# Kernel tuning notes

Hardware: AMD Instinct MI355X
Metric: run time of the kernel (lower is better)

## Reference

```python
import jax, jax.numpy as jnp
import numpy as np

GROUPS = 8
EPS = 1e-5


def group_norm(x, gamma, beta):
    # x: (b, c, h, w); normalize per sample over each group of c//GROUPS channels and all spatial dims
    b, c, h, w = x.shape
    xg = x.reshape(b, GROUPS, c // GROUPS, h, w)
    mean = jnp.mean(xg, axis=(2, 3, 4), keepdims=True)
    var = jnp.var(xg, axis=(2, 3, 4), keepdims=True)
    xn = ((xg - mean) * jax.lax.rsqrt(var + EPS)).reshape(b, c, h, w)
    return xn * gamma[None, :, None, None] + beta[None, :, None, None]


def setup_inputs() -> dict:
    key = jax.random.key(0)
    k1, k2, k3 = jax.random.split(key, 3)
    b, c, h, w = 32, 256, 32, 32
    x = jax.random.normal(k1, (b, c, h, w), dtype=jnp.float32)
    qkv_w = jax.random.normal(k2, (3 * c, c), dtype=jnp.float32) * 0.02
    qkv_b = jnp.zeros((3 * c,), dtype=jnp.float32)
    out_w = jax.random.normal(k3, (c, c), dtype=jnp.float32) * 0.02
    out_b = jnp.zeros((c,), dtype=jnp.float32)
    gn_gamma = jnp.ones((c,), dtype=jnp.float32)
    gn_beta = jnp.zeros((c,), dtype=jnp.float32)
    return {"x": x, "gn_gamma": gn_gamma, "gn_beta": gn_beta,
            "qkv_w": qkv_w, "qkv_b": qkv_b, "out_w": out_w, "out_b": out_b}


def reference(x, gn_gamma, gn_beta, qkv_w, qkv_b, out_w, out_b):
    b, c, h, w = x.shape
    xn = group_norm(x, gn_gamma, gn_beta)
    # 1x1 conv == per-pixel linear: (b,c,h,w) x (3c,c) -> (b,3c,h,w)
    qkv = jnp.einsum('bchw,dc->bdhw', xn, qkv_w) + qkv_b[None, :, None, None]
    q, k, v = jnp.split(qkv, 3, axis=1)
    # (b, c, h, w) -> (b, hw, c)
    def tok(t):
        return t.transpose(0, 2, 3, 1).reshape(b, h * w, c)
    q, k, v = tok(q), tok(k), tok(v)
    scale = 1.0 / jnp.sqrt(jnp.asarray(c, dtype=x.dtype))
    scores = jnp.einsum('bnc,bmc->bnm', q, k) * scale  # (b, hw, hw)
    attn = jax.nn.softmax(scores, axis=-1)
    out = jnp.einsum('bnm,bmc->bnc', attn, v)  # (b, hw, c)
    out = out.reshape(b, h, w, c).transpose(0, 3, 1, 2)  # (b, c, h, w)
    out = jnp.einsum('bchw,dc->bdhw', out, out_w) + out_b[None, :, None, None]
    return out + x
```

## Files before the change

kernel.cpp:

```cpp
#include <hip/hip_runtime.h>
#include <hip/hip_bf16.h>
#include <stdint.h>


typedef __bf16 bf16_t;
typedef __bf16 bf16x4 __attribute__((ext_vector_type(4)));
typedef __bf16 bf16x8 __attribute__((ext_vector_type(8)));
typedef float f32x4 __attribute__((ext_vector_type(4)));
typedef float f32x16 __attribute__((ext_vector_type(16)));
typedef _Float16 f16x4 __attribute__((ext_vector_type(4)));

#define MFMA32(a, b, c) __builtin_amdgcn_mfma_f32_32x32x16_bf16((a), (b), (c), 0, 0, 0)
#define GLL16(g, l)                                                                     \
    __builtin_amdgcn_global_load_lds((const __attribute__((address_space(1))) void*)(g), \
                                     (__attribute__((address_space(3))) void*)(l), 16, 0, 0)
#define WAITV8 asm volatile("s_waitcnt vmcnt(8)" ::: "memory")
#define WAITV0 asm volatile("s_waitcnt vmcnt(0)" ::: "memory")
#define WLG0   asm volatile("s_waitcnt lgkmcnt(0)" ::: "memory")
#define SBAR   __builtin_amdgcn_s_barrier()
#define SCH0   __builtin_amdgcn_sched_barrier(0)

#define QSCALE 0.0901684400555f

__device__ inline uint32_t pack2(float a, float b) {
    union { uint32_t u; __bf16 h[2]; } w;
    w.h[0] = (__bf16)a; w.h[1] = (__bf16)b;
    return w.u;
}

__global__ void cast_bf16(const float* __restrict__ s, bf16_t* __restrict__ d, int n) {
    for (int i = blockIdx.x * blockDim.x + threadIdx.x; i < n; i += gridDim.x * blockDim.x)
        d[i] = (bf16_t)s[i];
}

__global__ __launch_bounds__(256) void gn_kernel(const float* __restrict__ x,
                                                 const float* __restrict__ gamma,
                                                 const float* __restrict__ beta,
                                                 bf16_t* __restrict__ xn) {
    extern __shared__ char gsm[];
    float* red = (float*)(gsm + 65536);
    int bg = blockIdx.x, b = bg >> 3, g = bg & 7;
    const float* base = x + (size_t)(b * 256 + g * 32) * 1024;
    int tid = threadIdx.x;

    float s = 0.f, ss = 0.f;
    #pragma unroll 4
    for (int c = 0; c < 32; c++) {
        float4 v = *(const float4*)(base + c * 1024 + tid * 4);
        s += v.x + v.y + v.z + v.w;
        ss += v.x * v.x + v.y * v.y + v.z * v.z + v.w * v.w;
        f16x4 h = {(_Float16)v.x, (_Float16)v.y, (_Float16)v.z, (_Float16)v.w};
        *(f16x4*)(gsm + c * 2048 + ((tid * 8) ^ ((c & 7) << 4))) = h;
    }
    for (int off = 32; off; off >>= 1) { s += __shfl_down(s, off); ss += __shfl_down(ss, off); }
    if ((tid & 63) == 0) { red[tid >> 6] = s; red[4 + (tid >> 6)] = ss; }
    __syncthreads();
    float S = red[0] + red[1] + red[2] + red[3];
    float SS = red[4] + red[5] + red[6] + red[7];
    float mean = S * (1.0f / 32768.0f);
    float var = SS * (1.0f / 32768.0f) - mean * mean;
    float rstd = rsqrtf(var + 1e-5f);

    int c = tid & 31;
    float gam = gamma[g * 32 + c] * rstd;
    float bet = beta[g * 32 + c] - mean * gam;
    bf16_t* dst = xn + (size_t)(b * 1024) * 256 + g * 32 + c;
    #pragma unroll 4
    for (int it = 0; it < 128; it++) {
        int p = it * 8 + (tid >> 5);
        _Float16 hv = *(_Float16*)(gsm + c * 2048 + ((p * 2) ^ ((c & 7) << 4)));
        dst[(size_t)p * 256] = (bf16_t)((float)hv * gam + bet);
    }
}

__device__ inline void stage128(const char* src, char* dstLDS, int wv, int lane) {
    int r2 = lane >> 5, u = lane & 31;
    #pragma unroll
    for (int t = 0; t < 16; t++) {
        int row = t * 8 + wv * 2 + r2;
        GLL16(src + (size_t)row * 512 + ((u ^ (row & 7)) * 16), dstLDS + (t * 8 + wv * 2) * 512);
    }
}
__device__ inline bf16x8 lds_frag(const char* base, int row, int sl) {
    return *(const bf16x8*)(base + row * 512 + ((sl ^ (row & 7)) * 16));
}

__global__ __launch_bounds__(256) void gemm_qk(const bf16_t* __restrict__ xn,
                                               const bf16_t* __restrict__ wq,
                                               const float* __restrict__ qkv_b,
                                               bf16_t* __restrict__ qb,
                                               bf16_t* __restrict__ kb) {
    extern __shared__ char smem[];
    char* As = smem; char* Bs = smem + 65536;
    int tid = threadIdx.x, wv = tid >> 6, lane = tid & 63;
    int m0 = blockIdx.x * 128, n0 = blockIdx.y * 128;
    stage128((const char*)xn + (size_t)m0 * 512, As, wv, lane);
    stage128((const char*)wq + (size_t)n0 * 512, Bs, wv, lane);
    __syncthreads();

    int wr = wv >> 1, wc = wv & 1, l31 = lane & 31, hi = lane >> 5;
    f32x16 acc[2][2] = {};
    #pragma unroll
    for (int ks = 0; ks < 16; ks++) {
        int sl = ks * 2 + hi;
        bf16x8 a0 = lds_frag(As, wr * 64 + l31, sl);
        bf16x8 a1 = lds_frag(As, wr * 64 + 32 + l31, sl);
        bf16x8 b0 = lds_frag(Bs, wc * 64 + l31, sl);
        bf16x8 b1 = lds_frag(Bs, wc * 64 + 32 + l31, sl);
        acc[0][0] = MFMA32(a0, b0, acc[0][0]);
        acc[0][1] = MFMA32(a0, b1, acc[0][1]);
        acc[1][0] = MFMA32(a1, b0, acc[1][0]);
        acc[1][1] = MFMA32(a1, b1, acc[1][1]);
    }
    #pragma unroll
    for (int ms = 0; ms < 2; ms++)
        #pragma unroll
        for (int ns = 0; ns < 2; ns++) {
            int n = n0 + wc * 64 + ns * 32 + l31;
            float bias = qkv_b[n];
            bool isq = n < 256;
            float sc = isq ? QSCALE : 1.0f;
            bf16_t* dst = isq ? qb : kb;
            int d = isq ? n : n - 256;
            #pragma unroll
            for (int r = 0; r < 16; r++) {
                int m = m0 + wr * 64 + ms * 32 + (r & 3) + 8 * (r >> 2) + 4 * hi;
                dst[(size_t)m * 256 + d] = (bf16_t)((acc[ms][ns][r] + bias) * sc);
            }
        }
}

__global__ __launch_bounds__(256) void gemm_v(const bf16_t* __restrict__ xn,
                                              const bf16_t* __restrict__ wq,
                                              const float* __restrict__ qkv_b,
                                              bf16_t* __restrict__ vt) {
    extern __shared__ char smem[];
    char* As = smem; char* Bs = smem + 65536;
    int tid = threadIdx.x, wv = tid >> 6, lane = tid & 63;
    int d0 = blockIdx.x * 128, t0 = blockIdx.y * 128;
    stage128((const char*)wq + (size_t)(512 + d0) * 512, As, wv, lane);
    stage128((const char*)xn + (size_t)t0 * 512, Bs, wv, lane);
    __syncthreads();

    int wr = wv >> 1, wc = wv & 1, l31 = lane & 31, hi = lane >> 5;
    f32x16 acc[2][2] = {};
    #pragma unroll
    for (int ks = 0; ks < 16; ks++) {
        int sl = ks * 2 + hi;
        bf16x8 a0 = lds_frag(As, wr * 64 + l31, sl);
        bf16x8 a1 = lds_frag(As, wr * 64 + 32 + l31, sl);
        bf16x8 b0 = lds_frag(Bs, wc * 64 + l31, sl);
        bf16x8 b1 = lds_frag(Bs, wc * 64 + 32 + l31, sl);
        acc[0][0] = MFMA32(a0, b0, acc[0][0]);
        acc[0][1] = MFMA32(a0, b1, acc[0][1]);
        acc[1][0] = MFMA32(a1, b0, acc[1][0]);
        acc[1][1] = MFMA32(a1, b1, acc[1][1]);
    }
    #pragma unroll
    for (int ms = 0; ms < 2; ms++)
        #pragma unroll
        for (int ns = 0; ns < 2; ns++) {
            int tok0 = t0 + wc * 64 + ns * 32;
            #pragma unroll
            for (int r = 0; r < 16; r++) {
                int d = d0 + wr * 64 + ms * 32 + (r & 3) + 8 * (r >> 2) + 4 * hi;
                int tok = tok0 + l31;
                int bb = tok >> 10, pos = tok & 1023;
                vt[(size_t)bb * 262144 + (size_t)d * 1024 + pos] =
                    (bf16_t)(acc[ms][ns][r] + qkv_b[512 + d]);
            }
        }
}

__global__ __launch_bounds__(256) void gemm_out(const bf16_t* __restrict__ wo,
                                                const bf16_t* __restrict__ ao,
                                                const float* __restrict__ out_b,
                                                const float* __restrict__ x,
                                                float* __restrict__ out) {
    extern __shared__ char smem[];
    char* As = smem; char* Bs = smem + 65536;
    int tid = threadIdx.x, wv = tid >> 6, lane = tid & 63;
    int c0 = blockIdx.x * 128, t0 = blockIdx.y * 128;
    stage128((const char*)wo + (size_t)c0 * 512, As, wv, lane);
    stage128((const char*)ao + (size_t)t0 * 512, Bs, wv, lane);
    __syncthreads();

    int wr = wv >> 1, wc = wv & 1, l31 = lane & 31, hi = lane >> 5;
    f32x16 acc[2][2] = {};
    #pragma unroll
    for (int ks = 0; ks < 16; ks++) {
        int sl = ks * 2 + hi;
        bf16x8 a0 = lds_frag(As, wr * 64 + l31, sl);
        bf16x8 a1 = lds_frag(As, wr * 64 + 32 + l31, sl);
        bf16x8 b0 = lds_frag(Bs, wc * 64 + l31, sl);
        bf16x8 b1 = lds_frag(Bs, wc * 64 + 32 + l31, sl);
        acc[0][0] = MFMA32(a0, b0, acc[0][0]);
        acc[0][1] = MFMA32(a0, b1, acc[0][1]);
        acc[1][0] = MFMA32(a1, b0, acc[1][0]);
        acc[1][1] = MFMA32(a1, b1, acc[1][1]);
    }
    #pragma unroll
    for (int ms = 0; ms < 2; ms++)
        #pragma unroll
        for (int ns = 0; ns < 2; ns++) {
            #pragma unroll
            for (int r = 0; r < 16; r++) {
                int c = c0 + wr * 64 + ms * 32 + (r & 3) + 8 * (r >> 2) + 4 * hi;
                int tok = t0 + wc * 64 + ns * 32 + l31;
                int bb = tok >> 10, pos = tok & 1023;
                size_t idx = ((size_t)bb * 256 + c) * 1024 + pos;
                out[idx] = acc[ms][ns][r] + out_b[c] + x[idx];
            }
        }
}

__global__ __launch_bounds__(256, 1) void attn_kernel(const bf16_t* __restrict__ qb,
                                                      const bf16_t* __restrict__ kb,
                                                      const bf16_t* __restrict__ vt,
                                                      bf16_t* __restrict__ ao) {
    extern __shared__ char smem[];
    int tid = threadIdx.x, i = blockIdx.x;
    int b = (i & 7) + ((i >> 6) << 3);
    int qt = (i >> 3) & 7;
    int wv = tid >> 6, lane = tid & 63, l31 = lane & 31, hi = lane >> 5;

    const char* kbase = (const char*)kb + (size_t)b * 524288;
    const char* vbase = (const char*)vt + (size_t)b * 524288;

    int qg = qt * 128 + wv * 32 + l31;
    const char* qsrc = (const char*)qb + (size_t)(b * 1024 + qg) * 512;
    bf16x8 qf[16];
    #pragma unroll
    for (int ks = 0; ks < 16; ks++) qf[ks] = *(const bf16x8*)(qsrc + ks * 32 + hi * 16);

    f32x16 o[8] = {};
    f32x16 sp0 = {}, sp1 = {};
    float mrun = -1e30f, lrun = 0.f;

    auto stage_K = [&](int ch) {
        char* Kd = smem + (ch & 1) * 32768;
        int j0 = ch * 64;
        #pragma unroll
        for (int t = 0; t < 8; t++) {
            int r0 = wv * 16 + t * 2;
            int r = r0 + (lane >> 5), u = lane & 31;
            GLL16(kbase + (size_t)(j0 + r) * 512 + ((u ^ (r & 7)) * 16), Kd + r0 * 512);
        }
    };
    auto stage_V = [&](int ch) {
        char* Vd = smem + 65536 + (ch & 1) * 32768;
        int j0 = ch * 64;
        #pragma unroll
        for (int t = 0; t < 8; t++) {
            int r0 = wv * 64 + t * 8;
            int r = r0 + (lane >> 3), u = lane & 7;
            GLL16(vbase + (size_t)r * 2048 + j0 * 2 + ((u ^ (r & 7)) * 16), Vd + r0 * 128);
        }
    };
    auto qkt = [&](int ch, f32x16& s0, f32x16& s1) {
        const char* Ks = smem + (ch & 1) * 32768;
        #pragma unroll
        for (int ks = 0; ks < 16; ks++) {
            int col = ks * 32 + hi * 16;
            bf16x8 k0 = *(const bf16x8*)(Ks + l31 * 512 + (col ^ ((l31 & 7) << 4)));
            bf16x8 k1 = *(const bf16x8*)(Ks + (32 + l31) * 512 + (col ^ ((l31 & 7) << 4)));
            s0 = MFMA32(k0, qf[ks], s0);
            s1 = MFMA32(k1, qf[ks], s1);
        }
    };
    auto smax_pv = [&](int ch) {
        float mc = -1e30f;
        #pragma unroll
        for (int r = 0; r < 16; r++) mc = fmaxf(mc, fmaxf(sp0[r], sp1[r]));
        mc = fmaxf(mc, __shfl_xor(mc, 32));
        float mo = mrun;
        float mn = (mc <= mo + 8.0f) ? mo : mc;
        float rs = 0.f;
        #pragma unroll
        for (int r = 0; r < 16; r++) {
            sp0[r] = exp2f(sp0[r] - mn);
            sp1[r] = exp2f(sp1[r] - mn);
            rs += sp0[r] + sp1[r];
        }
        rs += __shfl_xor(rs, 32);
        float al = exp2f(mo - mn);
        lrun = lrun * al + rs;
        mrun = mn;
        if (__any(mn != mo)) {
            #pragma unroll
            for (int dt = 0; dt < 8; dt++) o[dt] = o[dt] * al;
        }
        const char* Vs = smem + 65536 + (ch & 1) * 32768;
        #pragma unroll
        for (int pk = 0; pk < 4; pk++) {
            float e0 = (pk < 2) ? sp0[(pk & 1) * 8 + 0] : sp1[(pk & 1) * 8 + 0];
            float e1 = (pk < 2) ? sp0[(pk & 1) * 8 + 1] : sp1[(pk & 1) * 8 + 1];
            float e2 = (pk < 2) ? sp0[(pk & 1) * 8 + 2] : sp1[(pk & 1) * 8 + 2];
            float e3 = (pk < 2) ? sp0[(pk & 1) * 8 + 3] : sp1[(pk & 1) * 8 + 3];
            float e4 = (pk < 2) ? sp0[(pk & 1) * 8 + 4] : sp1[(pk & 1) * 8 + 4];
            float e5 = (pk < 2) ? sp0[(pk & 1) * 8 + 5] : sp1[(pk & 1) * 8 + 5];
            float e6 = (pk < 2) ? sp0[(pk & 1) * 8 + 6] : sp1[(pk & 1) * 8 + 6];
            float e7 = (pk < 2) ? sp0[(pk & 1) * 8 + 7] : sp1[(pk & 1) * 8 + 7];
            uint32_t A0 = pack2(e0, e1), A1 = pack2(e2, e3);
            uint32_t B0 = pack2(e4, e5), B1 = pack2(e6, e7);
            asm volatile("v_permlane32_swap_b32 %0, %1" : "+v"(B0), "+v"(A0));
            asm volatile("v_permlane32_swap_b32 %0, %1" : "+v"(B1), "+v"(A1));
            union { bf16x8 v; uint32_t u[4]; } pw;
            pw.u[0] = A0; pw.u[1] = A1; pw.u[2] = B0; pw.u[3] = B1;
            #pragma unroll
            for (int dt = 0; dt < 8; dt++) {
                int d = dt * 32 + l31;
                bf16x8 vf =
                    *(const bf16x8*)(Vs + d * 128 + ((pk * 32 + hi * 16) ^ ((d & 7) << 4)));
                o[dt] = MFMA32(vf, pw.v, o[dt]);
            }
        }
    };

    stage_K(0); stage_V(0);
    WAITV8; SCH0; SBAR;
    stage_K(1);
    qkt(0, sp0, sp1);
    WLG0; SCH0; SBAR;
    stage_V(1);

    for (int ch = 1; ch < 16; ch++) {
        WAITV8; SCH0; SBAR;
        if (ch < 15) stage_K(ch + 1);
        f32x16 sn0 = {}, sn1 = {};
        qkt(ch, sn0, sn1);
        smax_pv(ch - 1);
        WLG0; SCH0; SBAR;
        if (ch < 15) stage_V(ch + 1);
        sp0 = sn0; sp1 = sn1;
    }
    WAITV0; SCH0; SBAR;
    smax_pv(15);

    float inv = 1.0f / lrun;
    char* aod = (char*)ao + (size_t)(b * 1024 + qg) * 512;
    #pragma unroll
    for (int dt = 0; dt < 8; dt++) {
        #pragma unroll
        for (int rg = 0; rg < 4; rg++) {
            bf16x4 w;
            #pragma unroll
            for (int r = 0; r < 4; r++) w[r] = (bf16_t)(o[dt][rg * 4 + r] * inv);
            *(bf16x4*)(aod + dt * 64 + rg * 16 + hi * 8) = w;
        }
    }
}

extern "C" void kernel_launch(void* const* d_in, const int* in_sizes, int n_in,
                              void* d_out, int out_size, void* d_ws, size_t ws_size,
                              hipStream_t stream) {
    (void)in_sizes; (void)n_in; (void)out_size; (void)ws_size;
    const float* x      = (const float*)d_in[0];
    const float* gamma  = (const float*)d_in[1];
    const float* beta   = (const float*)d_in[2];
    const float* qkv_w  = (const float*)d_in[3];
    const float* qkv_b  = (const float*)d_in[4];
    const float* out_w  = (const float*)d_in[5];
    const float* out_b  = (const float*)d_in[6];
    float* out = (float*)d_out;

    char* ws = (char*)d_ws;
    const size_t MB16 = 16777216;
    bf16_t* xn  = (bf16_t*)(ws);
    bf16_t* qb  = (bf16_t*)(ws + 1 * MB16);
    bf16_t* kb  = (bf16_t*)(ws + 2 * MB16);
    bf16_t* vt  = (bf16_t*)(ws + 3 * MB16);
    bf16_t* ao  = (bf16_t*)(ws + 4 * MB16);
    bf16_t* wqb = (bf16_t*)(ws + 5 * MB16);
    bf16_t* wob = (bf16_t*)(ws + 5 * MB16 + 393216);

    cast_bf16<<<192, 256, 0, stream>>>(qkv_w, wqb, 196608);
    cast_bf16<<<64, 256, 0, stream>>>(out_w, wob, 65536);
    gn_kernel<<<256, 256, 65600, stream>>>(x, gamma, beta, xn);
    gemm_qk<<<dim3(256, 4), 256, 131072, stream>>>(xn, wqb, qkv_b, qb, kb);
    gemm_v<<<dim3(2, 256), 256, 131072, stream>>>(xn, wqb, qkv_b, vt);
    attn_kernel<<<256, 256, 131072, stream>>>(qb, kb, vt, ao);
    gemm_out<<<dim3(2, 256), 256, 131072, stream>>>(wob, ao, out_b, x, out);
}
```

Before: 142.5 us.

## Fuse QKV GEMMs, restructure out GEMM, widen LDS swizzle, add MFMA priority

The separate Q/K and V projection kernels become one kernel per 128-token tile. It keeps the activation tile resident in LDS and streams double-buffered 64-row weight tiles. The output projection is restructured the same way, and the two weight casts are merged into one launch. LDS swizzles for K, V and the GEMMs change from 3-bit to 5-bit XOR patterns to reduce bank conflicts, and s_setprio brackets the MFMA loops. The goal is fewer launches, less redundant activation loading and fewer LDS conflicts. The cost is grids of only 256 blocks with one block per CU, plus serial per-block loops.

```diff
diff --git a/kernel.cpp b/kernel.cpp
--- a/kernel.cpp
+++ b/kernel.cpp
@@ -6,19 +6,17 @@
 typedef __bf16 bf16_t;
 typedef __bf16 bf16x4 __attribute__((ext_vector_type(4)));
 typedef __bf16 bf16x8 __attribute__((ext_vector_type(8)));
-typedef float f32x4 __attribute__((ext_vector_type(4)));
 typedef float f32x16 __attribute__((ext_vector_type(16)));
 typedef _Float16 f16x4 __attribute__((ext_vector_type(4)));
 
 #define MFMA32(a, b, c) __builtin_amdgcn_mfma_f32_32x32x16_bf16((a), (b), (c), 0, 0, 0)
-#define GLL16(g, l)                                                                     \
+#define GLL16(g, l)                                                                      \
     __builtin_amdgcn_global_load_lds((const __attribute__((address_space(1))) void*)(g), \
                                      (__attribute__((address_space(3))) void*)(l), 16, 0, 0)
 #define WAITV8 asm volatile("s_waitcnt vmcnt(8)" ::: "memory")
 #define WAITV0 asm volatile("s_waitcnt vmcnt(0)" ::: "memory")
 #define WLG0   asm volatile("s_waitcnt lgkmcnt(0)" ::: "memory")
 #define SBAR   __builtin_amdgcn_s_barrier()
-#define SCH0   __builtin_amdgcn_sched_barrier(0)
 
 #define QSCALE 0.0901684400555f
 
@@ -28,9 +26,12 @@
     return w.u;
 }
 
-__global__ void cast_bf16(const float* __restrict__ s, bf16_t* __restrict__ d, int n) {
-    for (int i = blockIdx.x * blockDim.x + threadIdx.x; i < n; i += gridDim.x * blockDim.x)
-        d[i] = (bf16_t)s[i];
+__global__ void cast_w(const float* __restrict__ s1, bf16_t* __restrict__ d1, int n1,
+                       const float* __restrict__ s2, bf16_t* __restrict__ d2, int n2) {
+    int i = blockIdx.x * blockDim.x + threadIdx.x;
+    int stride = gridDim.x * blockDim.x;
+    for (int k = i; k < n1; k += stride) d1[k] = (bf16_t)s1[k];
+    for (int k = i; k < n2; k += stride) d2[k] = (bf16_t)s2[k];
 }
 
 __global__ __launch_bounds__(256) void gn_kernel(const float* __restrict__ x,
@@ -73,145 +74,103 @@
     }
 }
 
-__device__ inline void stage128(const char* src, char* dstLDS, int wv, int lane) {
-    int r2 = lane >> 5, u = lane & 31;
-    #pragma unroll
-    for (int t = 0; t < 16; t++) {
-        int row = t * 8 + wv * 2 + r2;
-        GLL16(src + (size_t)row * 512 + ((u ^ (row & 7)) * 16), dstLDS + (t * 8 + wv * 2) * 512);
-    }
-}
-__device__ inline bf16x8 lds_frag(const char* base, int row, int sl) {
-    return *(const bf16x8*)(base + row * 512 + ((sl ^ (row & 7)) * 16));
-}
-
-__global__ __launch_bounds__(256) void gemm_qk(const bf16_t* __restrict__ xn,
-                                               const bf16_t* __restrict__ wq,
-                                               const float* __restrict__ qkv_b,
-                                               bf16_t* __restrict__ qb,
-                                               bf16_t* __restrict__ kb) {
+__global__ __launch_bounds__(256, 1) void gemm_qkv(const bf16_t* __restrict__ xn,
+                                                   const bf16_t* __restrict__ wq,
+                                                   const float* __restrict__ qkv_b,
+                                                   bf16_t* __restrict__ qb,
+                                                   bf16_t* __restrict__ kb,
+                                                   bf16_t* __restrict__ vt) {
     extern __shared__ char smem[];
-    char* As = smem; char* Bs = smem + 65536;
+    char* As = smem;
     int tid = threadIdx.x, wv = tid >> 6, lane = tid & 63;
-    int m0 = blockIdx.x * 128, n0 = blockIdx.y * 128;
-    stage128((const char*)xn + (size_t)m0 * 512, As, wv, lane);
-    stage128((const char*)wq + (size_t)n0 * 512, Bs, wv, lane);
-    __syncthreads();
-
-    int wr = wv >> 1, wc = wv & 1, l31 = lane & 31, hi = lane >> 5;
-    f32x16 acc[2][2] = {};
-    #pragma unroll
-    for (int ks = 0; ks < 16; ks++) {
-        int sl = ks * 2 + hi;
-        bf16x8 a0 = lds_frag(As, wr * 64 + l31, sl);
-        bf16x8 a1 = lds_frag(As, wr * 64 + 32 + l31, sl);
-        bf16x8 b0 = lds_frag(Bs, wc * 64 + l31, sl);
-        bf16x8 b1 = lds_frag(Bs, wc * 64 + 32 + l31, sl);
-        acc[0][0] = MFMA32(a0, b0, acc[0][0]);
-        acc[0][1] = MFMA32(a0, b1, acc[0][1]);
-        acc[1][0] = MFMA32(a1, b0, acc[1][0]);
-        acc[1][1] = MFMA32(a1, b1, acc[1][1]);
-    }
-    #pragma unroll
-    for (int ms = 0; ms < 2; ms++)
-        #pragma unroll
-        for (int ns = 0; ns < 2; ns++) {
-            int n = n0 + wc * 64 + ns * 32 + l31;
-            float bias = qkv_b[n];
-            bool isq = n < 256;
+    int l31 = lane & 31, hi = lane >> 5;
+    int t0 = blockIdx.x * 128;
+    const char* asrc = (const char*)xn + (size_t)t0 * 512;
+    const char* wsrc = (const char*)wq;
+
+    {
+        int u = lane & 31, rofs = lane >> 5;
+        #pragma unroll
+        for (int t = 0; t < 16; t++) {
+            int r0 = t * 8 + wv * 2;
+            int r = r0 + rofs;
+            GLL16(asrc + (size_t)r * 512 + ((u ^ (r & 31)) * 16), As + r0 * 512);
+        }
+    }
+    auto stage_B = [&](int nt) {
+        char* Bd = smem + 65536 + (nt & 1) * 32768;
+        int u = lane & 31, rofs = lane >> 5;
+        #pragma unroll
+        for (int t = 0; t < 8; t++) {
+            int r0 = wv * 16 + t * 2;
+            int r = r0 + rofs;
+            GLL16(wsrc + (size_t)(nt * 64 + r) * 512 + ((u ^ (r & 31)) * 16), Bd + r0 * 512);
+        }
+    };
+    stage_B(0);
+    WAITV0; SBAR;
+
+    int wm = wv >> 1, wd = wv & 1;
+    int bb = t0 >> 10, pos0 = t0 & 1023;
+
+    for (int nt = 0; nt < 12; nt++) {
+        if (nt < 11) stage_B(nt + 1);
+        const char* Bs = smem + 65536 + (nt & 1) * 32768;
+        f32x16 acc0 = {}, acc1 = {};
+        if (nt < 8) {
+            __builtin_amdgcn_s_setprio(1);
+            #pragma unroll
+            for (int ks = 0; ks < 16; ks++) {
+                int col = ks * 32 + hi * 16;
+                bf16x8 a0 = *(const bf16x8*)(As + (wm * 64 + l31) * 512 + (col ^ (l31 << 4)));
+                bf16x8 a1 = *(const bf16x8*)(As + (wm * 64 + 32 + l31) * 512 + (col ^ (l31 << 4)));
+                bf16x8 b  = *(const bf16x8*)(Bs + (wd * 32 + l31) * 512 + (col ^ (l31 << 4)));
+                acc0 = MFMA32(a0, b, acc0);
+                acc1 = MFMA32(a1, b, acc1);
+            }
+            __builtin_amdgcn_s_setprio(0);
+            int d = nt * 64 + wd * 32 + l31;
+            bool isq = nt < 4;
+            float bias = qkv_b[d];
+            bf16_t* dst = isq ? qb : kb;
+            int dd = isq ? d : d - 256;
             float sc = isq ? QSCALE : 1.0f;
-            bf16_t* dst = isq ? qb : kb;
-            int d = isq ? n : n - 256;
-            #pragma unroll
-            for (int r = 0; r < 16; r++) {
-                int m = m0 + wr * 64 + ms * 32 + (r & 3) + 8 * (r >> 2) + 4 * hi;
-                dst[(size_t)m * 256 + d] = (bf16_t)((acc[ms][ns][r] + bias) * sc);
-            }
-        }
-}
-
-__global__ __launch_bounds__(256) void gemm_v(const bf16_t* __restrict__ xn,
-                                              const bf16_t* __restrict__ wq,
-                                              const float* __restrict__ qkv_b,
-                                              bf16_t* __restrict__ vt) {
-    extern __shared__ char smem[];
-    char* As = smem; char* Bs = smem + 65536;
-    int tid = threadIdx.x, wv = tid >> 6, lane = tid & 63;
-    int d0 = blockIdx.x * 128, t0 = blockIdx.y * 128;
-    stage128((const char*)wq + (size_t)(512 + d0) * 512, As, wv, lane);
-    stage128((const char*)xn + (size_t)t0 * 512, Bs, wv, lane);
-    __syncthreads();
-
-    int wr = wv >> 1, wc = wv & 1, l31 = lane & 31, hi = lane >> 5;
-    f32x16 acc[2][2] = {};
-    #pragma unroll
-    for (int ks = 0; ks < 16; ks++) {
-        int sl = ks * 2 + hi;
-        bf16x8 a0 = lds_frag(As, wr * 64 + l31, sl);
-        bf16x8 a1 = lds_frag(As, wr * 64 + 32 + l31, sl);
-        bf16x8 b0 = lds_frag(Bs, wc * 64 + l31, sl);
-        bf16x8 b1 = lds_frag(Bs, wc * 64 + 32 + l31, sl);
-        acc[0][0] = MFMA32(a0, b0, acc[0][0]);
-        acc[0][1] = MFMA32(a0, b1, acc[0][1]);
-        acc[1][0] = MFMA32(a1, b0, acc[1][0]);
-        acc[1][1] = MFMA32(a1, b1, acc[1][1]);
-    }
-    #pragma unroll
-    for (int ms = 0; ms < 2; ms++)
-        #pragma unroll
-        for (int ns = 0; ns < 2; ns++) {
-            int tok0 = t0 + wc * 64 + ns * 32;
-            #pragma unroll
-            for (int r = 0; r < 16; r++) {
-                int d = d0 + wr * 64 + ms * 32 + (r & 3) + 8 * (r >> 2) + 4 * hi;
-                int tok = tok0 + l31;
-                int bb = tok >> 10, pos = tok & 1023;
-                vt[(size_t)bb * 262144 + (size_t)d * 1024 + pos] =
-                    (bf16_t)(acc[ms][ns][r] + qkv_b[512 + d]);
-            }
-        }
-}
-
-__global__ __launch_bounds__(256) void gemm_out(const bf16_t* __restrict__ wo,
-                                                const bf16_t* __restrict__ ao,
-                                                const float* __restrict__ out_b,
-                                                const float* __restrict__ x,
-                                                float* __restrict__ out) {
-    extern __shared__ char smem[];
-    char* As = smem; char* Bs = smem + 65536;
-    int tid = threadIdx.x, wv = tid >> 6, lane = tid & 63;
-    int c0 = blockIdx.x * 128, t0 = blockIdx.y * 128;
-    stage128((const char*)wo + (size_t)c0 * 512, As, wv, lane);
-    stage128((const char*)ao + (size_t)t0 * 512, Bs, wv, lane);
-    __syncthreads();
-
-    int wr = wv >> 1, wc = wv & 1, l31 = lane & 31, hi = lane >> 5;
-    f32x16 acc[2][2] = {};
-    #pragma unroll
-    for (int ks = 0; ks < 16; ks++) {
-        int sl = ks * 2 + hi;
-        bf16x8 a0 = lds_frag(As, wr * 64 + l31, sl);
-        bf16x8 a1 = lds_frag(As, wr * 64 + 32 + l31, sl);
-        bf16x8 b0 = lds_frag(Bs, wc * 64 + l31, sl);
-        bf16x8 b1 = lds_frag(Bs, wc * 64 + 32 + l31, sl);
-        acc[0][0] = MFMA32(a0, b0, acc[0][0]);
-        acc[0][1] = MFMA32(a0, b1, acc[0][1]);
-        acc[1][0] = MFMA32(a1, b0, acc[1][0]);
-        acc[1][1] = MFMA32(a1, b1, acc[1][1]);
-    }
-    #pragma unroll
-    for (int ms = 0; ms < 2; ms++)
-        #pragma unroll
-        for (int ns = 0; ns < 2; ns++) {
-            #pragma unroll
-            for (int r = 0; r < 16; r++) {
-                int c = c0 + wr * 64 + ms * 32 + (r & 3) + 8 * (r >> 2) + 4 * hi;
-                int tok = t0 + wc * 64 + ns * 32 + l31;
-                int bb = tok >> 10, pos = tok & 1023;
-                size_t idx = ((size_t)bb * 256 + c) * 1024 + pos;
-                out[idx] = acc[ms][ns][r] + out_b[c] + x[idx];
-            }
-        }
+            #pragma unroll
+            for (int ms = 0; ms < 2; ms++) {
+                #pragma unroll
+                for (int r = 0; r < 16; r++) {
+                    float v = ms ? acc1[r] : acc0[r];
+                    int tok = t0 + wm * 64 + ms * 32 + (r & 3) + 8 * (r >> 2) + 4 * hi;
+                    dst[(size_t)tok * 256 + dd] = (bf16_t)((v + bias) * sc);
+                }
+            }
+        } else {
+            __builtin_amdgcn_s_setprio(1);
+            #pragma unroll
+            for (int ks = 0; ks < 16; ks++) {
+                int col = ks * 32 + hi * 16;
+                bf16x8 a0 = *(const bf16x8*)(As + (wm * 64 + l31) * 512 + (col ^ (l31 << 4)));
+                bf16x8 a1 = *(const bf16x8*)(As + (wm * 64 + 32 + l31) * 512 + (col ^ (l31 << 4)));
+                bf16x8 b  = *(const bf16x8*)(Bs + (wd * 32 + l31) * 512 + (col ^ (l31 << 4)));
+                acc0 = MFMA32(b, a0, acc0);
+                acc1 = MFMA32(b, a1, acc1);
+            }
+            __builtin_amdgcn_s_setprio(0);
+            int dbase = (nt - 8) * 64 + wd * 32;
+            #pragma unroll
+            for (int ms = 0; ms < 2; ms++) {
+                int pos = pos0 + wm * 64 + ms * 32 + l31;
+                #pragma unroll
+                for (int r = 0; r < 16; r++) {
+                    float v = ms ? acc1[r] : acc0[r];
+                    int d = dbase + (r & 3) + 8 * (r >> 2) + 4 * hi;
+                    vt[(size_t)bb * 262144 + (size_t)d * 1024 + pos] =
+                        (bf16_t)(v + qkv_b[512 + d]);
+                }
+            }
+        }
+        if (nt < 11) { WAITV0; SBAR; }
+    }
 }
 
 __global__ __launch_bounds__(256, 1) void attn_kernel(const bf16_t* __restrict__ qb,
@@ -244,7 +203,7 @@
         for (int t = 0; t < 8; t++) {
             int r0 = wv * 16 + t * 2;
             int r = r0 + (lane >> 5), u = lane & 31;
-            GLL16(kbase + (size_t)(j0 + r) * 512 + ((u ^ (r & 7)) * 16), Kd + r0 * 512);
+            GLL16(kbase + (size_t)(j0 + r) * 512 + ((u ^ (r & 31)) * 16), Kd + r0 * 512);
         }
     };
     auto stage_V = [&](int ch) {
@@ -254,33 +213,37 @@
         for (int t = 0; t < 8; t++) {
             int r0 = wv * 64 + t * 8;
             int r = r0 + (lane >> 3), u = lane & 7;
-            GLL16(vbase + (size_t)r * 2048 + j0 * 2 + ((u ^ (r & 7)) * 16), Vd + r0 * 128);
+            int s5 = (((r & 3) << 3) | u) ^ ((r >> 2) & 31);
+            int d_src = (r & ~3) | (s5 >> 3);
+            GLL16(vbase + (size_t)d_src * 2048 + j0 * 2 + (s5 & 7) * 16, Vd + r0 * 128);
         }
     };
     auto qkt = [&](int ch, f32x16& s0, f32x16& s1) {
         const char* Ks = smem + (ch & 1) * 32768;
+        __builtin_amdgcn_s_setprio(1);
         #pragma unroll
         for (int ks = 0; ks < 16; ks++) {
             int col = ks * 32 + hi * 16;
-            bf16x8 k0 = *(const bf16x8*)(Ks + l31 * 512 + (col ^ ((l31 & 7) << 4)));
-            bf16x8 k1 = *(const bf16x8*)(Ks + (32 + l31) * 512 + (col ^ ((l31 & 7) << 4)));
+            bf16x8 k0 = *(const bf16x8*)(Ks + l31 * 512 + (col ^ (l31 << 4)));
+            bf16x8 k1 = *(const bf16x8*)(Ks + (32 + l31) * 512 + (col ^ (l31 << 4)));
             s0 = MFMA32(k0, qf[ks], s0);
             s1 = MFMA32(k1, qf[ks], s1);
         }
-    };
-    auto smax_pv = [&](int ch) {
+        __builtin_amdgcn_s_setprio(0);
+    };
+    auto smax_pv = [&](f32x16& t0v, f32x16& t1v, int ch) {
         float mc = -1e30f;
         #pragma unroll
-        for (int r = 0; r < 16; r++) mc = fmaxf(mc, fmaxf(sp0[r], sp1[r]));
+        for (int r = 0; r < 16; r++) mc = fmaxf(mc, fmaxf(t0v[r], t1v[r]));
         mc = fmaxf(mc, __shfl_xor(mc, 32));
         float mo = mrun;
         float mn = (mc <= mo + 8.0f) ? mo : mc;
         float rs = 0.f;
         #pragma unroll
         for (int r = 0; r < 16; r++) {
-            sp0[r] = exp2f(sp0[r] - mn);
-            sp1[r] = exp2f(sp1[r] - mn);
-            rs += sp0[r] + sp1[r];
+            t0v[r] = exp2f(t0v[r] - mn);
+            t1v[r] = exp2f(t1v[r] - mn);
+            rs += t0v[r] + t1v[r];
         }
         rs += __shfl_xor(rs, 32);
         float al = exp2f(mo - mn);
@@ -293,49 +256,51 @@
         const char* Vs = smem + 65536 + (ch & 1) * 32768;
         #pragma unroll
         for (int pk = 0; pk < 4; pk++) {
-            float e0 = (pk < 2) ? sp0[(pk & 1) * 8 + 0] : sp1[(pk & 1) * 8 + 0];
-            float e1 = (pk < 2) ? sp0[(pk & 1) * 8 + 1] : sp1[(pk & 1) * 8 + 1];
-            float e2 = (pk < 2) ? sp0[(pk & 1) * 8 + 2] : sp1[(pk & 1) * 8 + 2];
-            float e3 = (pk < 2) ? sp0[(pk & 1) * 8 + 3] : sp1[(pk & 1) * 8 + 3];
-            float e4 = (pk < 2) ? sp0[(pk & 1) * 8 + 4] : sp1[(pk & 1) * 8 + 4];
-            float e5 = (pk < 2) ? sp0[(pk & 1) * 8 + 5] : sp1[(pk & 1) * 8 + 5];
-            float e6 = (pk < 2) ? sp0[(pk & 1) * 8 + 6] : sp1[(pk & 1) * 8 + 6];
-            float e7 = (pk < 2) ? sp0[(pk & 1) * 8 + 7] : sp1[(pk & 1) * 8 + 7];
+            float e0 = (pk < 2) ? t0v[(pk & 1) * 8 + 0] : t1v[(pk & 1) * 8 + 0];
+            float e1 = (pk < 2) ? t0v[(pk & 1) * 8 + 1] : t1v[(pk & 1) * 8 + 1];
+            float e2 = (pk < 2) ? t0v[(pk & 1) * 8 + 2] : t1v[(pk & 1) * 8 + 2];
+            float e3 = (pk < 2) ? t0v[(pk & 1) * 8 + 3] : t1v[(pk & 1) * 8 + 3];
+            float e4 = (pk < 2) ? t0v[(pk & 1) * 8 + 4] : t1v[(pk & 1) * 8 + 4];
+            float e5 = (pk < 2) ? t0v[(pk & 1) * 8 + 5] : t1v[(pk & 1) * 8 + 5];
+            float e6 = (pk < 2) ? t0v[(pk & 1) * 8 + 6] : t1v[(pk & 1) * 8 + 6];
+            float e7 = (pk < 2) ? t0v[(pk & 1) * 8 + 7] : t1v[(pk & 1) * 8 + 7];
             uint32_t A0 = pack2(e0, e1), A1 = pack2(e2, e3);
             uint32_t B0 = pack2(e4, e5), B1 = pack2(e6, e7);
             asm volatile("v_permlane32_swap_b32 %0, %1" : "+v"(B0), "+v"(A0));
             asm volatile("v_permlane32_swap_b32 %0, %1" : "+v"(B1), "+v"(A1));
             union { bf16x8 v; uint32_t u[4]; } pw;
             pw.u[0] = A0; pw.u[1] = A1; pw.u[2] = B0; pw.u[3] = B1;
+            __builtin_amdgcn_s_setprio(1);
             #pragma unroll
             for (int dt = 0; dt < 8; dt++) {
                 int d = dt * 32 + l31;
-                bf16x8 vf =
-                    *(const bf16x8*)(Vs + d * 128 + ((pk * 32 + hi * 16) ^ ((d & 7) << 4)));
+                int a = (d * 128 + pk * 32 + hi * 16) ^ (((d >> 2) & 31) << 4);
+                bf16x8 vf = *(const bf16x8*)(Vs + a);
                 o[dt] = MFMA32(vf, pw.v, o[dt]);
             }
+            __builtin_amdgcn_s_setprio(0);
         }
     };
 
     stage_K(0); stage_V(0);
-    WAITV8; SCH0; SBAR;
+    WAITV8; SBAR;
     stage_K(1);
     qkt(0, sp0, sp1);
-    WLG0; SCH0; SBAR;
+    WLG0; SBAR;
     stage_V(1);
 
     for (int ch = 1; ch < 16; ch++) {
-        WAITV8; SCH0; SBAR;
+        WAITV8; SBAR;
         if (ch < 15) stage_K(ch + 1);
         f32x16 sn0 = {}, sn1 = {};
         qkt(ch, sn0, sn1);
-        smax_pv(ch - 1);
-        WLG0; SCH0; SBAR;
+        smax_pv(sp0, sp1, ch - 1);
+        WLG0; SBAR;
         if (ch < 15) stage_V(ch + 1);
         sp0 = sn0; sp1 = sn1;
     }
-    WAITV0; SCH0; SBAR;
-    smax_pv(15);
+    WAITV0; SBAR;
+    smax_pv(sp0, sp1, 15);
 
     float inv = 1.0f / lrun;
     char* aod = (char*)ao + (size_t)(b * 1024 + qg) * 512;
@@ -348,6 +313,74 @@
             for (int r = 0; r < 4; r++) w[r] = (bf16_t)(o[dt][rg * 4 + r] * inv);
             *(bf16x4*)(aod + dt * 64 + rg * 16 + hi * 8) = w;
         }
+    }
+}
+
+__global__ __launch_bounds__(256, 1) void gemm_out(const bf16_t* __restrict__ wo,
+                                                   const bf16_t* __restrict__ ao,
+                                                   const float* __restrict__ out_b,
+                                                   const float* __restrict__ x,
+                                                   float* __restrict__ out) {
+    extern __shared__ char smem[];
+    char* Bs = smem;
+    int tid = threadIdx.x, wv = tid >> 6, lane = tid & 63;
+    int l31 = lane & 31, hi = lane >> 5;
+    int t0 = blockIdx.x * 128;
+    const char* bsrc = (const char*)ao + (size_t)t0 * 512;
+    const char* wsrc = (const char*)wo;
+
+    {
+        int u = lane & 31, rofs = lane >> 5;
+        #pragma unroll
+        for (int t = 0; t < 16; t++) {
+            int r0 = t * 8 + wv * 2;
+            int r = r0 + rofs;
+            GLL16(bsrc + (size_t)r * 512 + ((u ^ (r & 31)) * 16), Bs + r0 * 512);
+        }
+    }
+    auto stage_W = [&](int ct) {
+        char* Wd = smem + 65536 + (ct & 1) * 32768;
+        int u = lane & 31, rofs = lane >> 5;
+        #pragma unroll
+        for (int t = 0; t < 8; t++) {
+            int r0 = wv * 16 + t * 2;
+            int r = r0 + rofs;
+            GLL16(wsrc + (size_t)(ct * 64 + r) * 512 + ((u ^ (r & 31)) * 16), Wd + r0 * 512);
+        }
+    };
+    stage_W(0);
+    WAITV0; SBAR;
+
+    int wm = wv >> 1, wc = wv & 1;
+    int bb = t0 >> 10, pos0 = t0 & 1023;
+
+    for (int ct = 0; ct < 4; ct++) {
+        if (ct < 3) stage_W(ct + 1);
+        const char* Ws = smem + 65536 + (ct & 1) * 32768;
+        f32x16 acc0 = {}, acc1 = {};
+        __builtin_amdgcn_s_setprio(1);
+        #pragma unroll
+        for (int ks = 0; ks < 16; ks++) {
+            int col = ks * 32 + hi * 16;
+            bf16x8 w  = *(const bf16x8*)(Ws + (wc * 32 + l31) * 512 + (col ^ (l31 << 4)));
+            bf16x8 b0 = *(const bf16x8*)(Bs + (wm * 64 + l31) * 512 + (col ^ (l31 << 4)));
+            bf16x8 b1 = *(const bf16x8*)(Bs + (wm * 64 + 32 + l31) * 512 + (col ^ (l31 << 4)));
+            acc0 = MFMA32(w, b0, acc0);
+            acc1 = MFMA32(w, b1, acc1);
+        }
+        __builtin_amdgcn_s_setprio(0);
+        #pragma unroll
+        for (int ms = 0; ms < 2; ms++) {
+            int pos = pos0 + wm * 64 + ms * 32 + l31;
+            #pragma unroll
+            for (int r = 0; r < 16; r++) {
+                float v = ms ? acc1[r] : acc0[r];
+                int c = ct * 64 + wc * 32 + (r & 3) + 8 * (r >> 2) + 4 * hi;
+                size_t idx = ((size_t)bb * 256 + c) * 1024 + pos;
+                out[idx] = v + out_b[c] + x[idx];
+            }
+        }
+        if (ct < 3) { WAITV0; SBAR; }
     }
 }
 
@@ -374,11 +407,9 @@
     bf16_t* wqb = (bf16_t*)(ws + 5 * MB16);
     bf16_t* wob = (bf16_t*)(ws + 5 * MB16 + 393216);
 
-    cast_bf16<<<192, 256, 0, stream>>>(qkv_w, wqb, 196608);
-    cast_bf16<<<64, 256, 0, stream>>>(out_w, wob, 65536);
+    cast_w<<<256, 256, 0, stream>>>(qkv_w, wqb, 196608, out_w, wob, 65536);
     gn_kernel<<<256, 256, 65600, stream>>>(x, gamma, beta, xn);
-    gemm_qk<<<dim3(256, 4), 256, 131072, stream>>>(xn, wqb, qkv_b, qb, kb);
-    gemm_v<<<dim3(2, 256), 256, 131072, stream>>>(xn, wqb, qkv_b, vt);
+    gemm_qkv<<<256, 256, 131072, stream>>>(xn, wqb, qkv_b, qb, kb, vt);
     attn_kernel<<<256, 256, 131072, stream>>>(qb, kb, vt, ao);
-    gemm_out<<<dim3(2, 256), 256, 131072, stream>>>(wob, ao, out_b, x, out);
-}
+    gemm_out<<<256, 256, 131072, stream>>>(wob, ao, out_b, x, out);
+}
```

Measured after the change: 138.7 us. 2.7% less time.
